# Performance work log

Hardware: AMD Instinct MI355X
Metric: run time of the kernel (lower is better)

## Reference

```python
import jax, jax.numpy as jnp
import numpy as np

N = 20000      # nodes
E = 320000     # edges
D = 512        # width
L = 4          # layers
VOCAB = 256
MAX_POS = 256
EPS = 1e-5


def setup_inputs() -> dict:
    key = jax.random.key(0)
    ks = jax.random.split(key, 12)
    tokens = jax.random.randint(ks[0], (N,), 0, VOCAB)
    pos = jax.random.randint(ks[1], (N,), 0, MAX_POS)
    edge_index = jax.random.randint(ks[2], (2, E), 0, N)
    vocab_emb = jax.random.normal(ks[3], (VOCAB, D), jnp.float32) * 0.05
    pos_emb = jax.random.normal(ks[4], (MAX_POS, D), jnp.float32) * 0.05
    bn_gamma = jnp.ones((L, D), jnp.float32)
    bn_beta = jnp.zeros((L, D), jnp.float32)
    bn_mean = jax.random.normal(ks[5], (L, D), jnp.float32) * 0.1
    bn_var = jax.random.uniform(ks[6], (L, D), jnp.float32, 0.5, 1.5)
    W_rel = jax.random.normal(ks[7], (L, D, D), jnp.float32) * (1.0 / np.sqrt(D))
    b_rel = jnp.zeros((L, D), jnp.float32)
    W_root = jax.random.normal(ks[8], (L, D, D), jnp.float32) * (1.0 / np.sqrt(D))
    return {
        "tokens": tokens, "pos": pos, "edge_index": edge_index,
        "vocab_emb": vocab_emb, "pos_emb": pos_emb,
        "bn_gamma": bn_gamma, "bn_beta": bn_beta,
        "bn_mean": bn_mean, "bn_var": bn_var,
        "W_rel": W_rel, "b_rel": b_rel, "W_root": W_root,
    }


def reference(tokens, pos, edge_index, vocab_emb, pos_emb,
              bn_gamma, bn_beta, bn_mean, bn_var, W_rel, b_rel, W_root):
    src, dst = edge_index[0], edge_index[1]
    # in-degree for mean aggregation (clamped to 1 like PyG mean aggr)
    deg = jax.ops.segment_sum(jnp.ones((E,), jnp.float32), dst, num_segments=N)
    deg = jnp.maximum(deg, 1.0)[:, None]                     # [N,1]

    x = vocab_emb[tokens] + pos_emb[pos]                     # [N,D]
    for l in range(L):
        # BatchNorm1d, eval mode with running stats
        inv = bn_gamma[l] * jax.lax.rsqrt(bn_var[l] + EPS)
        x = (x - bn_mean[l]) * inv + bn_beta[l]
        # GraphConv: W_root x_i + W_rel * mean_{j->i} x_j + b
        agg = jax.ops.segment_sum(x[src], dst, num_segments=N) / deg
        x = agg @ W_rel[l].T + b_rel[l] + x @ W_root[l].T
        x = jax.nn.relu(x)
    return x
```

## Files before the change

### kernel.cpp

```cpp
#include <hip/hip_runtime.h>
#include <cstdint>

#define EPS 1e-5f

typedef __attribute__((ext_vector_type(8))) short bf16x8;
typedef __attribute__((ext_vector_type(4))) float f32x4;
typedef __attribute__((ext_vector_type(4))) unsigned int u32x4;

__device__ __forceinline__ unsigned short f2bf(float x) {
    uint32_t u = __float_as_uint(x);
    u += 0x7fffu + ((u >> 16) & 1u);
    return (unsigned short)(u >> 16);
}
__device__ __forceinline__ uint32_t pack2(float lo, float hi) {
    return (uint32_t)f2bf(lo) | ((uint32_t)f2bf(hi) << 16);
}
__device__ __forceinline__ float bflo(uint32_t p) { return __uint_as_float(p << 16); }
__device__ __forceinline__ float bfhi(uint32_t p) { return __uint_as_float(p & 0xffff0000u); }

__device__ __forceinline__ void async_ld16(const void* g, const void* l) {
    __builtin_amdgcn_global_load_lds(
        (const __attribute__((address_space(1))) uint32_t*)(uintptr_t)g,
        (__attribute__((address_space(3))) uint32_t*)(uint32_t)(uintptr_t)l,
        16, 0, 0);
}

__global__ __launch_bounds__(256) void count_kernel(const int* __restrict__ ei,
                                                    int* __restrict__ deg, int E) {
    int e = blockIdx.x * 256 + threadIdx.x;
    if (e < E) atomicAdd(&deg[ei[E + e]], 1);
}

__global__ __launch_bounds__(1024) void scan_kernel(const int* __restrict__ deg,
                                                    int* __restrict__ offsets,
                                                    int* __restrict__ cursor, int N) {
    extern __shared__ int sm[];
    int* sdeg = sm;
    int* part = sm + ((N + 1023) & ~1023);
    const int t = threadIdx.x;
    const int CH = (N + 1023) >> 10;
    for (int j = t; j < N; j += 1024) sdeg[j] = deg[j];
    __syncthreads();
    const int base = t * CH;
    int s = 0;
    for (int j = 0; j < CH; ++j) {
        int idx = base + j;
        if (idx < N) s += sdeg[idx];
    }
    part[t] = s;
    __syncthreads();
    for (int off = 1; off < 1024; off <<= 1) {
        int add = (t >= off) ? part[t - off] : 0;
        __syncthreads();
        part[t] += add;
        __syncthreads();
    }
    int run = (t == 0) ? 0 : part[t - 1];
    for (int j = 0; j < CH; ++j) {
        int idx = base + j;
        if (idx < N) {
            int dgi = sdeg[idx];
            sdeg[idx] = run;
            run += dgi;
        }
    }
    __syncthreads();
    for (int j = t; j < N; j += 1024) {
        int v = sdeg[j];
        offsets[j] = v;
        cursor[j]  = v;
    }
    if (t == 1023) offsets[N] = run;
}

__global__ __launch_bounds__(256) void fill_kernel(const int* __restrict__ ei,
                                                   int* __restrict__ cursor,
                                                   int* __restrict__ csr, int E) {
    int e = blockIdx.x * 256 + threadIdx.x;
    if (e < E) {
        int dd = ei[E + e];
        int slot = atomicAdd(&cursor[dd], 1);
        csr[slot] = ei[e];
    }
}

__global__ __launch_bounds__(256) void embed_bn_kernel(const int* __restrict__ tok,
                                                       const int* __restrict__ pos,
                                                       const float* __restrict__ vemb,
                                                       const float* __restrict__ pemb,
                                                       const float* __restrict__ gamma,
                                                       const float* __restrict__ beta,
                                                       const float* __restrict__ mean,
                                                       const float* __restrict__ var,
                                                       uint32_t* __restrict__ Acat, int N) {
    const int idx = blockIdx.x * 256 + threadIdx.x;
    if (idx >= N * 128) return;
    const int row = idx >> 7;
    const int c = (idx & 127) * 4;
    const int tk = tok[row];
    const int ps = pos[row];
    const float4 a = *(const float4*)&vemb[(size_t)tk * 512 + c];
    const float4 b = *(const float4*)&pemb[(size_t)ps * 512 + c];
    const float4 g = *(const float4*)&gamma[c];
    const float4 be = *(const float4*)&beta[c];
    const float4 mn = *(const float4*)&mean[c];
    const float4 vr = *(const float4*)&var[c];
    const float y0 = (a.x + b.x - mn.x) * (g.x * rsqrtf(vr.x + EPS)) + be.x;
    const float y1 = (a.y + b.y - mn.y) * (g.y * rsqrtf(vr.y + EPS)) + be.y;
    const float y2 = (a.z + b.z - mn.z) * (g.z * rsqrtf(vr.z + EPS)) + be.z;
    const float y3 = (a.w + b.w - mn.w) * (g.w * rsqrtf(vr.w + EPS)) + be.w;
    uint2 o;
    o.x = pack2(y0, y1);
    o.y = pack2(y2, y3);
    *(uint2*)&Acat[(size_t)row * 512 + (c >> 1)] = o;
}

__global__ __launch_bounds__(256) void castW_kernel(const float* __restrict__ Wroot,
                                                    const float* __restrict__ Wrel,
                                                    uint32_t* __restrict__ Wcat) {
    const int p = blockIdx.x * 256 + threadIdx.x;
    const int o  = p >> 9;
    const int dp = p & 511;
    float2 v;
    if (dp < 256) v = *(const float2*)&Wroot[(size_t)o * 512 + dp * 2];
    else          v = *(const float2*)&Wrel[(size_t)o * 512 + (dp - 256) * 2];
    Wcat[(size_t)o * 512 + dp] = pack2(v.x, v.y);
}

__global__ __launch_bounds__(256) void castW4_kernel(const float* __restrict__ Wroot,
                                                     const float* __restrict__ Wrel,
                                                     uint32_t* __restrict__ Wcat4) {
    const int p = blockIdx.x * 256 + threadIdx.x;
    const int l   = p >> 18;
    const int rem = p & 262143;
    const int o   = rem >> 9;
    const int dp  = rem & 511;
    float2 v;
    if (dp < 256) v = *(const float2*)&Wroot[(size_t)l * 262144 + (size_t)o * 512 + dp * 2];
    else          v = *(const float2*)&Wrel[(size_t)l * 262144 + (size_t)o * 512 + (dp - 256) * 2];
    Wcat4[(size_t)l * 262144 + (size_t)o * 512 + dp] = pack2(v.x, v.y);
}

__global__ __launch_bounds__(256) void aggregate_kernel(uint32_t* __restrict__ Acat,
                                                        const int* __restrict__ offsets,
                                                        const int* __restrict__ csr,
                                                        int N) {
    const int node = blockIdx.x * 4 + (threadIdx.x >> 6);
    if (node >= N) return;
    const int lane = threadIdx.x & 63;
    const int col = lane * 4;
    const int beg = offsets[node];
    const int end = offsets[node + 1];
    float s[8] = {0.f, 0.f, 0.f, 0.f, 0.f, 0.f, 0.f, 0.f};
    int e = beg;
    for (; e + 8 <= end; e += 8) {
        const int i0 = csr[e];
        const int i1 = csr[e + 1];
        const int i2 = csr[e + 2];
        const int i3 = csr[e + 3];
        const int i4 = csr[e + 4];
        const int i5 = csr[e + 5];
        const int i6 = csr[e + 6];
        const int i7 = csr[e + 7];
        const uint4 p0 = *(const uint4*)&Acat[(size_t)i0 * 512 + col];
        const uint4 p1 = *(const uint4*)&Acat[(size_t)i1 * 512 + col];
        const uint4 p2 = *(const uint4*)&Acat[(size_t)i2 * 512 + col];
        const uint4 p3 = *(const uint4*)&Acat[(size_t)i3 * 512 + col];
        const uint4 p4 = *(const uint4*)&Acat[(size_t)i4 * 512 + col];
        const uint4 p5 = *(const uint4*)&Acat[(size_t)i5 * 512 + col];
        const uint4 p6 = *(const uint4*)&Acat[(size_t)i6 * 512 + col];
        const uint4 p7 = *(const uint4*)&Acat[(size_t)i7 * 512 + col];
        s[0] += (bflo(p0.x) + bflo(p1.x)) + (bflo(p2.x) + bflo(p3.x))
              + (bflo(p4.x) + bflo(p5.x)) + (bflo(p6.x) + bflo(p7.x));
        s[1] += (bfhi(p0.x) + bfhi(p1.x)) + (bfhi(p2.x) + bfhi(p3.x))
              + (bfhi(p4.x) + bfhi(p5.x)) + (bfhi(p6.x) + bfhi(p7.x));
        s[2] += (bflo(p0.y) + bflo(p1.y)) + (bflo(p2.y) + bflo(p3.y))
              + (bflo(p4.y) + bflo(p5.y)) + (bflo(p6.y) + bflo(p7.y));
        s[3] += (bfhi(p0.y) + bfhi(p1.y)) + (bfhi(p2.y) + bfhi(p3.y))
              + (bfhi(p4.y) + bfhi(p5.y)) + (bfhi(p6.y) + bfhi(p7.y));
        s[4] += (bflo(p0.z) + bflo(p1.z)) + (bflo(p2.z) + bflo(p3.z))
              + (bflo(p4.z) + bflo(p5.z)) + (bflo(p6.z) + bflo(p7.z));
        s[5] += (bfhi(p0.z) + bfhi(p1.z)) + (bfhi(p2.z) + bfhi(p3.z))
              + (bfhi(p4.z) + bfhi(p5.z)) + (bfhi(p6.z) + bfhi(p7.z));
        s[6] += (bflo(p0.w) + bflo(p1.w)) + (bflo(p2.w) + bflo(p3.w))
              + (bflo(p4.w) + bflo(p5.w)) + (bflo(p6.w) + bflo(p7.w));
        s[7] += (bfhi(p0.w) + bfhi(p1.w)) + (bfhi(p2.w) + bfhi(p3.w))
              + (bfhi(p4.w) + bfhi(p5.w)) + (bfhi(p6.w) + bfhi(p7.w));
    }
    for (; e + 4 <= end; e += 4) {
        const int i0 = csr[e];
        const int i1 = csr[e + 1];
        const int i2 = csr[e + 2];
        const int i3 = csr[e + 3];
        const uint4 p0 = *(const uint4*)&Acat[(size_t)i0 * 512 + col];
        const uint4 p1 = *(const uint4*)&Acat[(size_t)i1 * 512 + col];
        const uint4 p2 = *(const uint4*)&Acat[(size_t)i2 * 512 + col];
        const uint4 p3 = *(const uint4*)&Acat[(size_t)i3 * 512 + col];
        s[0] += bflo(p0.x) + bflo(p1.x) + bflo(p2.x) + bflo(p3.x);
        s[1] += bfhi(p0.x) + bfhi(p1.x) + bfhi(p2.x) + bfhi(p3.x);
        s[2] += bflo(p0.y) + bflo(p1.y) + bflo(p2.y) + bflo(p3.y);
        s[3] += bfhi(p0.y) + bfhi(p1.y) + bfhi(p2.y) + bfhi(p3.y);
        s[4] += bflo(p0.z) + bflo(p1.z) + bflo(p2.z) + bflo(p3.z);
        s[5] += bfhi(p0.z) + bfhi(p1.z) + bfhi(p2.z) + bfhi(p3.z);
        s[6] += bflo(p0.w) + bflo(p1.w) + bflo(p2.w) + bflo(p3.w);
        s[7] += bfhi(p0.w) + bfhi(p1.w) + bfhi(p2.w) + bfhi(p3.w);
    }
    for (; e < end; ++e) {
        const int i0 = csr[e];
        const uint4 p0 = *(const uint4*)&Acat[(size_t)i0 * 512 + col];
        s[0] += bflo(p0.x); s[1] += bfhi(p0.x);
        s[2] += bflo(p0.y); s[3] += bfhi(p0.y);
        s[4] += bflo(p0.z); s[5] += bfhi(p0.z);
        s[6] += bflo(p0.w); s[7] += bfhi(p0.w);
    }
    const int dgi = end - beg;
    const float inv = 1.0f / (float)(dgi > 0 ? dgi : 1);
    u32x4 o;
    o.x = pack2(s[0] * inv, s[1] * inv);
    o.y = pack2(s[2] * inv, s[3] * inv);
    o.z = pack2(s[4] * inv, s[5] * inv);
    o.w = pack2(s[6] * inv, s[7] * inv);
    __builtin_nontemporal_store(o, (u32x4*)&Acat[(size_t)node * 512 + 256 + col]);
}

__global__ __launch_bounds__(256) void gemm_bt_bias_relu(const unsigned short* __restrict__ A,
                                                         const unsigned short* __restrict__ B,
                                                         const float* __restrict__ bias,
                                                         const float* __restrict__ gamma,
                                                         const float* __restrict__ beta,
                                                         const float* __restrict__ mean,
                                                         const float* __restrict__ var,
                                                         int last,
                                                         float* __restrict__ C,
                                                         unsigned short* __restrict__ Abn,
                                                         int M, int mt, int rpx) {
    __shared__ __align__(16) unsigned short As[128 * 32];
    __shared__ __align__(16) unsigned short Bs[128 * 32];

    const int bid = blockIdx.x;
    const int bm  = (bid & 7) * rpx + ((bid >> 3) >> 2);
    const int bn  = (bid >> 3) & 3;
    if (bm >= mt) return;

    const int t    = threadIdx.x;
    const int lane = t & 63;
    const int wave = t >> 6;
    const int wm = (wave >> 1) * 64;
    const int wn = (wave & 1) * 64;

    const int r  = t >> 2;
    const int kc = t & 3;
    const int kg = kc ^ ((r >> 1) & 3);
    int ar0 = bm * 128 + r;      if (ar0 >= M) ar0 = M - 1;
    int ar1 = bm * 128 + r + 64; if (ar1 >= M) ar1 = M - 1;
    const int br0 = bn * 128 + r;
    const int br1 = br0 + 64;

    const unsigned short* ga0 = A + (size_t)ar0 * 1024 + kg * 8;
    const unsigned short* ga1 = A + (size_t)ar1 * 1024 + kg * 8;
    const unsigned short* gb0 = B + (size_t)br0 * 1024 + kg * 8;
    const unsigned short* gb1 = B + (size_t)br1 * 1024 + kg * 8;

    unsigned short* la0 = &As[r * 32 + kc * 8];
    unsigned short* la1 = &As[(r + 64) * 32 + kc * 8];
    unsigned short* lb0 = &Bs[r * 32 + kc * 8];
    unsigned short* lb1 = &Bs[(r + 64) * 32 + kc * 8];

    const f32x4 zero = {0.f, 0.f, 0.f, 0.f};
    f32x4 acc[4][4];
#pragma unroll
    for (int i = 0; i < 4; ++i)
#pragma unroll
        for (int j = 0; j < 4; ++j) acc[i][j] = zero;

    const int lm = lane & 15;
    const int q  = lane >> 4;
    const int qs = (q ^ ((lm >> 1) & 3)) * 8;

    for (int k0 = 0; k0 < 1024; k0 += 32) {
        async_ld16(ga0 + k0, la0);
        async_ld16(ga1 + k0, la1);
        async_ld16(gb0 + k0, lb0);
        async_ld16(gb1 + k0, lb1);
        __syncthreads();

        bf16x8 afr[4], bfr[4];
#pragma unroll
        for (int mt2 = 0; mt2 < 4; ++mt2)
            afr[mt2] = *(const bf16x8*)&As[(wm + mt2 * 16 + lm) * 32 + qs];
#pragma unroll
        for (int nt = 0; nt < 4; ++nt)
            bfr[nt] = *(const bf16x8*)&Bs[(wn + nt * 16 + lm) * 32 + qs];
#pragma unroll
        for (int mt2 = 0; mt2 < 4; ++mt2)
#pragma unroll
            for (int nt = 0; nt < 4; ++nt)
                acc[mt2][nt] = __builtin_amdgcn_mfma_f32_16x16x32_bf16(afr[mt2], bfr[nt],
                                                                       acc[mt2][nt], 0, 0, 0);
        __syncthreads();
    }

#pragma unroll
    for (int nt = 0; nt < 4; ++nt) {
        const int col = bn * 128 + wn + nt * 16 + lm;
        const float bv = bias[col];
        float bn_inv = 0.f, bn_mb = 0.f;
        if (!last) {
            bn_inv = gamma[col] * rsqrtf(var[col] + EPS);
            bn_mb  = mean[col];
        }
        const float bn_beta = last ? 0.f : beta[col];
#pragma unroll
        for (int mt2 = 0; mt2 < 4; ++mt2) {
            const int row0 = bm * 128 + wm + mt2 * 16 + q * 4;
#pragma unroll
            for (int i = 0; i < 4; ++i) {
                const int row = row0 + i;
                if (row < M) {
                    float v = acc[mt2][nt][i] + bv;
                    v = v > 0.f ? v : 0.f;
                    if (last) {
                        C[(size_t)row * 512 + col] = v;
                    } else {
                        const float y = (v - bn_mb) * bn_inv + bn_beta;
                        Abn[(size_t)row * 1024 + col] = f2bf(y);
                    }
                }
            }
        }
    }
}

extern "C" void kernel_launch(void* const* d_in, const int* in_sizes, int n_in,
                              void* d_out, int out_size, void* d_ws, size_t ws_size,
                              hipStream_t stream) {
    const int*   tokens = (const int*)d_in[0];
    const int*   posi   = (const int*)d_in[1];
    const int*   ei     = (const int*)d_in[2];
    const float* vemb   = (const float*)d_in[3];
    const float* pemb   = (const float*)d_in[4];
    const float* gamma  = (const float*)d_in[5];
    const float* beta   = (const float*)d_in[6];
    const float* mean   = (const float*)d_in[7];
    const float* var    = (const float*)d_in[8];
    const float* Wrel   = (const float*)d_in[9];
    const float* brel   = (const float*)d_in[10];
    const float* Wroot  = (const float*)d_in[11];

    const int N = in_sizes[0];
    const int E = in_sizes[2] / 2;
    float* out = (float*)d_out;

    char* w = (char*)d_ws;
    int*      deg     = (int*)(w);
    int*      offsets = (int*)(w + 80000);
    int*      cursor  = (int*)(w + 160016);
    int*      csr     = (int*)(w + 320048);
    uint32_t* Acat    = (uint32_t*)(w + 1600064);
    uint32_t* Wcat    = (uint32_t*)(w + 42560064);

    const int batched = (ws_size >= 46754368ull) ? 1 : 0;

    const int scan_lds = (((N + 1023) & ~1023) + 1024) * 4;
    static bool s_attr = false;
    if (!s_attr) {
        (void)hipFuncSetAttribute(reinterpret_cast<const void*>(scan_kernel),
                                  hipFuncAttributeMaxDynamicSharedMemorySize, 163840);
        s_attr = true;
    }

    (void)hipMemsetAsync(deg, 0, (size_t)N * 4, stream);
    count_kernel<<<(E + 255) / 256, 256, 0, stream>>>(ei, deg, E);
    scan_kernel<<<1, 1024, scan_lds, stream>>>(deg, offsets, cursor, N);
    fill_kernel<<<(E + 255) / 256, 256, 0, stream>>>(ei, cursor, csr, E);

    embed_bn_kernel<<<(N * 128 + 255) / 256, 256, 0, stream>>>(
        tokens, posi, vemb, pemb, gamma, beta, mean, var, Acat, N);

    if (batched)
        castW4_kernel<<<4096, 256, 0, stream>>>(Wroot, Wrel, Wcat);

    const int mt  = (N + 127) >> 7;
    const int rpx = (mt + 7) >> 3;
    const int gb  = 8 * rpx * 4;

    for (int l = 0; l < 4; ++l) {
        const int last = (l == 3);
        if (!batched)
            castW_kernel<<<1024, 256, 0, stream>>>(Wroot + (size_t)l * 262144,
                                                   Wrel + (size_t)l * 262144, Wcat);
        aggregate_kernel<<<(N + 3) / 4, 256, 0, stream>>>(Acat, offsets, csr, N);
        const uint32_t* Wl = batched ? (Wcat + (size_t)l * 262144) : Wcat;
        gemm_bt_bias_relu<<<gb, 256, 0, stream>>>(
            (const unsigned short*)Acat, (const unsigned short*)Wl, brel + l * 512,
            gamma + (l + 1) * 512, beta + (l + 1) * 512,
            mean + (l + 1) * 512, var + (l + 1) * 512,
            last, out, (unsigned short*)Acat, N, mt, rpx);
    }
}
```

Baseline: 524.9 us.

## Double-buffer GEMM LDS tiles to overlap async loads with MFMA

```diff
diff --git a/kernel.cpp b/kernel.cpp
--- a/kernel.cpp
+++ b/kernel.cpp
@@ -234,8 +234,8 @@
                                                          float* __restrict__ C,
                                                          unsigned short* __restrict__ Abn,
                                                          int M, int mt, int rpx) {
-    __shared__ __align__(16) unsigned short As[128 * 32];
-    __shared__ __align__(16) unsigned short Bs[128 * 32];
+    __shared__ __align__(16) unsigned short As[2][128 * 32];
+    __shared__ __align__(16) unsigned short Bs[2][128 * 32];
 
     const int bid = blockIdx.x;
     const int bm  = (bid & 7) * rpx + ((bid >> 3) >> 2);
@@ -261,10 +261,8 @@
     const unsigned short* gb0 = B + (size_t)br0 * 1024 + kg * 8;
     const unsigned short* gb1 = B + (size_t)br1 * 1024 + kg * 8;
 
-    unsigned short* la0 = &As[r * 32 + kc * 8];
-    unsigned short* la1 = &As[(r + 64) * 32 + kc * 8];
-    unsigned short* lb0 = &Bs[r * 32 + kc * 8];
-    unsigned short* lb1 = &Bs[(r + 64) * 32 + kc * 8];
+    const int lofA0 = r * 32 + kc * 8;
+    const int lofA1 = (r + 64) * 32 + kc * 8;
 
     const f32x4 zero = {0.f, 0.f, 0.f, 0.f};
     f32x4 acc[4][4];
@@ -277,27 +275,38 @@
     const int q  = lane >> 4;
     const int qs = (q ^ ((lm >> 1) & 3)) * 8;
 
-    for (int k0 = 0; k0 < 1024; k0 += 32) {
-        async_ld16(ga0 + k0, la0);
-        async_ld16(ga1 + k0, la1);
-        async_ld16(gb0 + k0, lb0);
-        async_ld16(gb1 + k0, lb1);
-        __syncthreads();
-
+    async_ld16(ga0, &As[0][lofA0]);
+    async_ld16(ga1, &As[0][lofA1]);
+    async_ld16(gb0, &Bs[0][lofA0]);
+    async_ld16(gb1, &Bs[0][lofA1]);
+
+#pragma unroll 2
+    for (int ks = 0; ks < 32; ++ks) {
+        const int cur = ks & 1;
+        const int nxt = cur ^ 1;
+        asm volatile("s_waitcnt vmcnt(0)" ::: "memory");
+        __builtin_amdgcn_s_barrier();
+        __builtin_amdgcn_sched_barrier(0);
+        if (ks < 31) {
+            const int k1 = (ks + 1) * 32;
+            async_ld16(ga0 + k1, &As[nxt][lofA0]);
+            async_ld16(ga1 + k1, &As[nxt][lofA1]);
+            async_ld16(gb0 + k1, &Bs[nxt][lofA0]);
+            async_ld16(gb1 + k1, &Bs[nxt][lofA1]);
+        }
         bf16x8 afr[4], bfr[4];
 #pragma unroll
         for (int mt2 = 0; mt2 < 4; ++mt2)
-            afr[mt2] = *(const bf16x8*)&As[(wm + mt2 * 16 + lm) * 32 + qs];
+            afr[mt2] = *(const bf16x8*)&As[cur][(wm + mt2 * 16 + lm) * 32 + qs];
 #pragma unroll
         for (int nt = 0; nt < 4; ++nt)
-            bfr[nt] = *(const bf16x8*)&Bs[(wn + nt * 16 + lm) * 32 + qs];
+            bfr[nt] = *(const bf16x8*)&Bs[cur][(wn + nt * 16 + lm) * 32 + qs];
 #pragma unroll
         for (int mt2 = 0; mt2 < 4; ++mt2)
 #pragma unroll
             for (int nt = 0; nt < 4; ++nt)
                 acc[mt2][nt] = __builtin_amdgcn_mfma_f32_16x16x32_bf16(afr[mt2], bfr[nt],
                                                                        acc[mt2][nt], 0, 0, 0);
-        __syncthreads();
     }
 
 #pragma unroll
```

After: 508.3 us. -3.2%, faster.

## Triple-buffer GEMM LDS tiles with async prefetch two k-steps ahead

Applied to the files above, without the earlier changes.

```diff
diff --git a/kernel.cpp b/kernel.cpp
--- a/kernel.cpp
+++ b/kernel.cpp
@@ -234,8 +234,8 @@
                                                          float* __restrict__ C,
                                                          unsigned short* __restrict__ Abn,
                                                          int M, int mt, int rpx) {
-    __shared__ __align__(16) unsigned short As[128 * 32];
-    __shared__ __align__(16) unsigned short Bs[128 * 32];
+    __shared__ __align__(16) unsigned short As[3][128 * 32];
+    __shared__ __align__(16) unsigned short Bs[3][128 * 32];
 
     const int bid = blockIdx.x;
     const int bm  = (bid & 7) * rpx + ((bid >> 3) >> 2);
@@ -261,10 +261,8 @@
     const unsigned short* gb0 = B + (size_t)br0 * 1024 + kg * 8;
     const unsigned short* gb1 = B + (size_t)br1 * 1024 + kg * 8;
 
-    unsigned short* la0 = &As[r * 32 + kc * 8];
-    unsigned short* la1 = &As[(r + 64) * 32 + kc * 8];
-    unsigned short* lb0 = &Bs[r * 32 + kc * 8];
-    unsigned short* lb1 = &Bs[(r + 64) * 32 + kc * 8];
+    const int lofA0 = r * 32 + kc * 8;
+    const int lofA1 = (r + 64) * 32 + kc * 8;
 
     const f32x4 zero = {0.f, 0.f, 0.f, 0.f};
     f32x4 acc[4][4];
@@ -277,28 +275,44 @@
     const int q  = lane >> 4;
     const int qs = (q ^ ((lm >> 1) & 3)) * 8;
 
-    for (int k0 = 0; k0 < 1024; k0 += 32) {
-        async_ld16(ga0 + k0, la0);
-        async_ld16(ga1 + k0, la1);
-        async_ld16(gb0 + k0, lb0);
-        async_ld16(gb1 + k0, lb1);
-        __syncthreads();
-
-        bf16x8 afr[4], bfr[4];
-#pragma unroll
-        for (int mt2 = 0; mt2 < 4; ++mt2)
-            afr[mt2] = *(const bf16x8*)&As[(wm + mt2 * 16 + lm) * 32 + qs];
-#pragma unroll
-        for (int nt = 0; nt < 4; ++nt)
-            bfr[nt] = *(const bf16x8*)&Bs[(wn + nt * 16 + lm) * 32 + qs];
-#pragma unroll
-        for (int mt2 = 0; mt2 < 4; ++mt2)
-#pragma unroll
-            for (int nt = 0; nt < 4; ++nt)
-                acc[mt2][nt] = __builtin_amdgcn_mfma_f32_16x16x32_bf16(afr[mt2], bfr[nt],
-                                                                       acc[mt2][nt], 0, 0, 0);
-        __syncthreads();
-    }
+#define STAGE(KT, BUF) do {                                        \
+        const int koff = (KT) * 32;                                \
+        async_ld16(ga0 + koff, &As[BUF][lofA0]);                   \
+        async_ld16(ga1 + koff, &As[BUF][lofA1]);                   \
+        async_ld16(gb0 + koff, &Bs[BUF][lofA0]);                   \
+        async_ld16(gb1 + koff, &Bs[BUF][lofA1]);                   \
+    } while (0)
+
+#define GSTEP(CURB, STGB, KS, WLIT, DOSTG) do {                                 \
+        asm volatile("s_waitcnt vmcnt(" WLIT ")" ::: "memory");                 \
+        __builtin_amdgcn_s_barrier();                                           \
+        __builtin_amdgcn_sched_barrier(0);                                      \
+        if (DOSTG) STAGE((KS) + 2, STGB);                                       \
+        bf16x8 afr[4], bfr[4];                                                  \
+        _Pragma("unroll") for (int mt2 = 0; mt2 < 4; ++mt2)                     \
+            afr[mt2] = *(const bf16x8*)&As[CURB][(wm + mt2 * 16 + lm) * 32 + qs]; \
+        _Pragma("unroll") for (int nt = 0; nt < 4; ++nt)                        \
+            bfr[nt] = *(const bf16x8*)&Bs[CURB][(wn + nt * 16 + lm) * 32 + qs]; \
+        _Pragma("unroll") for (int mt2 = 0; mt2 < 4; ++mt2)                     \
+            _Pragma("unroll") for (int nt = 0; nt < 4; ++nt)                    \
+                acc[mt2][nt] = __builtin_amdgcn_mfma_f32_16x16x32_bf16(         \
+                    afr[mt2], bfr[nt], acc[mt2][nt], 0, 0, 0);                  \
+    } while (0)
+
+    STAGE(0, 0);
+    STAGE(1, 1);
+
+    for (int g = 0; g < 10; ++g) {
+        const int k0 = g * 3;
+        GSTEP(0, 2, k0 + 0, "4", 1);
+        GSTEP(1, 0, k0 + 1, "4", 1);
+        GSTEP(2, 1, k0 + 2, "4", 1);
+    }
+    GSTEP(0, 2, 30, "4", 0);
+    GSTEP(1, 2, 31, "0", 0);
+
+#undef STAGE
+#undef GSTEP
 
 #pragma unroll
     for (int nt = 0; nt < 4; ++nt) {
```

After: 551.9 us. 1.05x slower.
